# Optimization experiments

Hardware: AMD Instinct MI355X
Metric: run time of the kernel (lower is better)

The kernel has to match this reference:

```python
import jax, jax.numpy as jnp
import numpy as np

N, MA, F, NF = 512, 64, 128, 16
UPDATE_RATIO = 0.1
DECAY = 1.0
EPS = 1e-12  # avoids NaN grad of sqrt at self-distance 0 (torch diagonal is masked out by exp anyway)


def setup_inputs() -> dict:
    key = jax.random.key(0)
    ks = jax.random.split(key, 8)
    z = jax.random.randint(ks[0], (N, MA), 0, 10, dtype=jnp.int64) if jax.config.jax_enable_x64 else jax.random.randint(ks[0], (N, MA), 0, 10, dtype=jnp.int32)
    # pad last few atoms of each molecule with -1 to exercise the mask
    z = z.at[:, MA - 8:].set(-1)
    r = jax.random.normal(ks[1], (N, MA, 3), dtype=jnp.float32) * 3.0
    h = jax.random.normal(ks[2], (N, MA, F), dtype=jnp.float32)
    distances = jnp.linspace(0.5, 6.0, NF, dtype=jnp.float32)
    widths = jax.random.uniform(ks[3], (NF,), dtype=jnp.float32) * 0.5 + 0.5  # keep sigma > 0
    din = F * (1 + NF)  # 2176
    W1 = jax.random.normal(ks[4], (din, 512), dtype=jnp.float32) * (1.0 / np.sqrt(din))
    b1 = jnp.zeros((512,), dtype=jnp.float32)
    W2 = jax.random.normal(ks[5], (512, F), dtype=jnp.float32) * (1.0 / np.sqrt(512.0))
    b2 = jnp.zeros((F,), dtype=jnp.float32)
    return {"z": z, "r": r, "h": h, "distances": distances, "widths": widths,
            "W1": W1, "b1": b1, "W2": W2, "b2": b2}


def reference(z, r, h, distances, widths, W1, b1, W2, b2):
    n, ma = z.shape
    nf = distances.shape[0]
    # pairwise distance: (n, ma, ma)
    dv = r[:, :, None, :] - r[:, None, :, :]
    d = jnp.sqrt(jnp.sum(dv * dv, axis=-1) + EPS)
    mu = distances.reshape(1, nf, 1, 1)
    sigma = widths.reshape(1, nf, 1, 1)
    mask1 = (z > -1).astype(h.dtype)                      # (n, ma)
    pair_mask = mask1[:, :, None] * mask1[:, None, :]     # (n, ma, ma)
    # Gaussian RBF scores, masked: (n, nf, ma, ma)
    w = pair_mask[:, None] * jnp.exp(-((d[:, None] - mu) ** 2) / sigma) * 5.0
    # aggregate neighbor features: (n, ma, nf, F) -> (n, ma, nf*F)
    u = jnp.einsum('nfab,nbc->nafc', w, h).reshape(n, ma, nf * h.shape[-1])
    v = jnp.concatenate([h, u], axis=2)                   # (n, ma, F*(1+nf))
    v = jax.nn.silu(v @ W1 + b1) @ W2 + b2                # MLP 'net'
    h_new = h + v * UPDATE_RATIO * DECAY * mask1[:, :, None]
    return (z, r, h_new)
```

## Files before the change

### kernel.cpp

```cpp
#include <hip/hip_runtime.h>

#define MA 64
#define F 128
#define NF 16
#define HID 512
#define LDUB 144
#define LDWB 144
#define LDT1B 1040
#define UB0 0
#define UB1 9216
#define WL0 18432
#define WL1 27648

typedef float  float4v __attribute__((ext_vector_type(4)));
typedef short  short8  __attribute__((ext_vector_type(8)));
typedef int    int8v   __attribute__((ext_vector_type(8)));

static __device__ __forceinline__ unsigned int pack2bf(float x, float y) {
    unsigned int a = __float_as_uint(x) + 0x8000u;
    unsigned int b = __float_as_uint(y) + 0x8000u;
    return __builtin_amdgcn_perm(b, a, 0x07060302u);
}
static __device__ __forceinline__ unsigned short f2bf1(float x) {
    return (unsigned short)((__float_as_uint(x) + 0x8000u) >> 16);
}
static __device__ __forceinline__ unsigned int pk4fp8(float a, float b, float c, float d) {
    int p = __builtin_amdgcn_cvt_pk_fp8_f32(a, b, 0, false);
    p = __builtin_amdgcn_cvt_pk_fp8_f32(c, d, p, true);
    return (unsigned int)p;
}

#define LGKM_BAR() do {                                        \
    asm volatile("s_waitcnt lgkmcnt(0)" ::: "memory");         \
    __builtin_amdgcn_s_barrier();                              \
    asm volatile("" ::: "memory");                             \
} while (0)

__global__ void pack_frags(const float* __restrict__ W1, const float* __restrict__ W2,
                           unsigned char* __restrict__ w1p, unsigned short* __restrict__ w2p) {
    int gid  = blockIdx.x * 4 + (threadIdx.x >> 6);
    int lane = threadIdx.x & 63;
    int arow = lane & 15;
    int kq   = lane >> 4;
    if (gid < 544) {
        int kt = gid >> 5, jt = gid & 31;
        const float* base = W1 + (size_t)(kt * 128 + kq * 32) * HID + jt * 16 + arow;
        unsigned int o[8];
        #pragma unroll
        for (int p = 0; p < 8; p++)
            o[p] = pk4fp8(base[(p * 4 + 0) * HID], base[(p * 4 + 1) * HID],
                          base[(p * 4 + 2) * HID], base[(p * 4 + 3) * HID]);
        unsigned char* dst = w1p + ((size_t)gid * 64 + lane) * 32;
        *(uint4*)dst        = (uint4){o[0], o[1], o[2], o[3]};
        *(uint4*)(dst + 16) = (uint4){o[4], o[5], o[6], o[7]};
    } else if (gid < 544 + 128) {
        int g2 = gid - 544;
        int kt = g2 >> 3, mt = g2 & 7;
        const float* base = W2 + (size_t)(kt * 32 + kq * 8) * F + mt * 16 + arow;
        short8 o;
        #pragma unroll
        for (int j = 0; j < 8; j++) o[j] = (short)f2bf1(base[j * F]);
        *(short8*)(w2p + ((size_t)g2 * 64 + lane) * 8) = o;
    }
}

__launch_bounds__(512, 2)
__global__ void node_conv_mfma(const int* __restrict__ z, const float* __restrict__ rr,
        const float* __restrict__ h, const float* __restrict__ dist,
        const float* __restrict__ wid, const float* __restrict__ b1,
        const float* __restrict__ b2,
        const unsigned char* __restrict__ w1p, const unsigned short* __restrict__ w2p,
        float* __restrict__ out) {
    const int n = blockIdx.x;
    const int tid = threadIdx.x;
    const int lane = tid & 63;
    const int wave = tid >> 6;
    const int arow = lane & 15;
    const int quad = lane >> 4;
    const int kgrp = quad * 8;

    __shared__ __attribute__((aligned(16))) unsigned char lds[66560];
    __shared__ float r_lds[MA][5];

    const int N = gridDim.x;
    const float* hg = h + (size_t)n * MA * F;

    if (tid < MA) {
        int zi = z[n * MA + tid];
        out[(size_t)n * MA + tid] = (float)zi;
        r_lds[tid][0] = rr[(n * MA + tid) * 3 + 0];
        r_lds[tid][1] = rr[(n * MA + tid) * 3 + 1];
        r_lds[tid][2] = rr[(n * MA + tid) * 3 + 2];
        r_lds[tid][3] = (zi > -1) ? 1.0f : 0.0f;
    }
    if (tid < MA * 3)
        out[(size_t)N * MA + (size_t)n * MA * 3 + tid] = rr[(size_t)n * MA * 3 + tid];

    for (int i = tid; i < MA * F / 4; i += 512) {
        float4 v = ((const float4*)hg)[i];
        int a = i >> 5, c4 = (i & 31) * 4;
        *(unsigned int*)&lds[UB0 + a * LDUB + c4] = pk4fp8(v.x, v.y, v.z, v.w);
    }
    short8 ah[2];
    {
        int c = wave * 16 + arow;
        #pragma unroll
        for (int ks2 = 0; ks2 < 2; ks2++)
            #pragma unroll
            for (int j = 0; j < 8; j++)
                ah[ks2][j] = (short)f2bf1(hg[(size_t)(ks2 * 32 + kgrp + j) * F + c]);
    }
    __syncthreads();

    const int wa = tid >> 3;
    const int wb0 = (tid & 7) * 8;
    float dpre[8];
    {
        float ax = r_lds[wa][0], ay = r_lds[wa][1], az = r_lds[wa][2];
        float am = r_lds[wa][3];
        #pragma unroll
        for (int j = 0; j < 8; j++) {
            float dx = ax - r_lds[wb0 + j][0];
            float dy = ay - r_lds[wb0 + j][1];
            float dz = az - r_lds[wb0 + j][2];
            float d = sqrtf(dx * dx + dy * dy + dz * dz + 1e-12f);
            float mm = am * r_lds[wb0 + j][3];
            dpre[j] = d + (1.0f - mm) * 1e4f;
        }
    }

    {
        float mu = dist[0];
        float isg = 1.0f / wid[0];
        float e[8];
        #pragma unroll
        for (int j = 0; j < 8; j++) {
            float t = dpre[j] - mu;
            e[j] = 5.0f * __expf(-t * t * isg);
        }
        uint4 wp = { pack2bf(e[0], e[1]), pack2bf(e[2], e[3]),
                     pack2bf(e[4], e[5]), pack2bf(e[6], e[7]) };
        *(uint4*)&lds[WL0 + wa * LDWB + wb0 * 2] = wp;
    }
    int8v afr[4];
    #pragma unroll
    for (int mt = 0; mt < 4; mt++)
        afr[mt] = *(const int8v*)(w1p + ((size_t)((wave * 4 + mt) * 64 + lane)) * 32);
    LGKM_BAR();

    const float4v zf = {0.f, 0.f, 0.f, 0.f};
    float4v acc[4][4];
    #pragma unroll
    for (int i = 0; i < 4; i++)
        #pragma unroll
        for (int jv = 0; jv < 4; jv++) acc[i][jv] = zf;

    for (int f = 0; f <= NF; f++) {
        const int sel = f & 1;
        const int ubR = sel ? UB1 : UB0;
        const int ubW = sel ? UB0 : UB1;
        const int wlR = sel ? WL1 : WL0;
        const int wlW = sel ? WL0 : WL1;

        #pragma unroll
        for (int at = 0; at < 4; at++) {
            int8v bfr = *(const int8v*)&lds[ubR + (at * 16 + arow) * LDUB + quad * 32];
            #pragma unroll
            for (int mt = 0; mt < 4; mt++)
                acc[mt][at] = __builtin_amdgcn_mfma_scale_f32_16x16x128_f8f6f4(
                    afr[mt], bfr, acc[mt][at], 0, 0, 0, 127, 0, 127);
        }

        if (f < NF) {
            const unsigned char* pN = w1p + ((size_t)(((f + 1) * 32 + wave * 4) * 64 + lane)) * 32;
            #pragma unroll
            for (int mt = 0; mt < 4; mt++) afr[mt] = *(const int8v*)(pN + mt * 2048);

            float4v ud[4];
            #pragma unroll
            for (int at = 0; at < 4; at++) ud[at] = zf;
            #pragma unroll
            for (int ks2 = 0; ks2 < 2; ks2++)
                #pragma unroll
                for (int at = 0; at < 4; at++) {
                    short8 bw = *(const short8*)&lds[wlR + (at * 16 + arow) * LDWB + (ks2 * 32 + kgrp) * 2];
                    ud[at] = __builtin_amdgcn_mfma_f32_16x16x32_bf16(ah[ks2], bw, ud[at], 0, 0, 0);
                }
            #pragma unroll
            for (int at = 0; at < 4; at++) {
                unsigned int udp = pk4fp8(ud[at][0], ud[at][1], ud[at][2], ud[at][3]);
                *(unsigned int*)&lds[ubW + (at * 16 + arow) * LDUB + wave * 16 + quad * 4] = udp;
            }

            if (f <= NF - 2) {
                float mu = dist[f + 1];
                float isg = 1.0f / wid[f + 1];
                float e[8];
                #pragma unroll
                for (int j = 0; j < 8; j++) {
                    float t = dpre[j] - mu;
                    e[j] = 5.0f * __expf(-t * t * isg);
                }
                uint4 wp = { pack2bf(e[0], e[1]), pack2bf(e[2], e[3]),
                             pack2bf(e[4], e[5]), pack2bf(e[6], e[7]) };
                *(uint4*)&lds[wlW + wa * LDWB + wb0 * 2] = wp;
            }
        }
        LGKM_BAR();
    }

    float4 b1v[4];
    #pragma unroll
    for (int mt = 0; mt < 4; mt++)
        b1v[mt] = *(const float4*)&b1[wave * 64 + mt * 16 + quad * 4];

    short8 aw2r[16];
    #pragma unroll
    for (int ks = 0; ks < 16; ks++)
        aw2r[ks] = *(const short8*)(w2p + ((size_t)(ks * 8 + wave) * 64 + lane) * 8);

    #pragma unroll
    for (int mt = 0; mt < 4; mt++) {
        #pragma unroll
        for (int at = 0; at < 4; at++) {
            float xs[4];
            #pragma unroll
            for (int r = 0; r < 4; r++) {
                float x = acc[mt][at][r] + ((const float*)&b1v[mt])[r];
                xs[r] = x / (1.0f + __expf(-x));
            }
            uint2 pv = { pack2bf(xs[0], xs[1]), pack2bf(xs[2], xs[3]) };
            *(uint2*)&lds[(at * 16 + arow) * LDT1B + (wave * 64 + mt * 16 + quad * 4) * 2] = pv;
        }
    }
    LGKM_BAR();

    float4v g2[4];
    const float4v zf2 = {0.f, 0.f, 0.f, 0.f};
    #pragma unroll
    for (int n2 = 0; n2 < 4; n2++) g2[n2] = zf2;
    #pragma unroll
    for (int ks = 0; ks < 16; ks++) {
        #pragma unroll
        for (int n2 = 0; n2 < 4; n2++) {
            short8 bt = *(const short8*)&lds[(n2 * 16 + arow) * LDT1B + (ks * 32 + kgrp) * 2];
            g2[n2] = __builtin_amdgcn_mfma_f32_16x16x32_bf16(aw2r[ks], bt, g2[n2], 0, 0, 0);
        }
    }

    float* outh = out + (size_t)N * MA * 4 + (size_t)n * MA * F;
    const int c0 = wave * 16 + quad * 4;
    float4 b2v = *(const float4*)&b2[c0];
    #pragma unroll
    for (int n2 = 0; n2 < 4; n2++) {
        int a = n2 * 16 + arow;
        float m = r_lds[a][3] * 0.1f;
        float4 hv = *(const float4*)&hg[a * F + c0];
        float4 res;
        res.x = hv.x + (g2[n2][0] + b2v.x) * m;
        res.y = hv.y + (g2[n2][1] + b2v.y) * m;
        res.z = hv.z + (g2[n2][2] + b2v.z) * m;
        res.w = hv.w + (g2[n2][3] + b2v.w) * m;
        *(float4*)&outh[(size_t)a * F + c0] = res;
    }
}

extern "C" void kernel_launch(void* const* d_in, const int* in_sizes, int n_in,
                              void* d_out, int out_size, void* d_ws, size_t ws_size,
                              hipStream_t stream) {
    const int*   z    = (const int*)d_in[0];
    const float* rr   = (const float*)d_in[1];
    const float* h    = (const float*)d_in[2];
    const float* dist = (const float*)d_in[3];
    const float* wid  = (const float*)d_in[4];
    const float* W1   = (const float*)d_in[5];
    const float* b1   = (const float*)d_in[6];
    const float* W2   = (const float*)d_in[7];
    const float* b2   = (const float*)d_in[8];
    float* out = (float*)d_out;

    int Nmol = in_sizes[0] / MA;

    unsigned char*  w1p = (unsigned char*)d_ws;
    unsigned short* w2p = (unsigned short*)(w1p + (size_t)544 * 64 * 32);

    pack_frags<<<168, 256, 0, stream>>>(W1, W2, w1p, w2p);
    node_conv_mfma<<<Nmol, 512, 0, stream>>>(z, rr, h, dist, wid, b1, b2, w1p, w2p, out);
}
```

Measured before the change: 145.7 us.

## Cut register pressure by streaming weight fragments and raising the launch-bounds occupancy target

Raises the launch-bounds minimum blocks per CU from 2 to 4, which caps VGPRs per thread. To fit that cap, W1 FP8 fragments are now held two at a time (reloaded mid-iteration), the bias-free W2 fragments are double-buffered per k-step instead of 16 preloaded registers, and the feature-aggregation MFMAs are processed in pairs. The goal is more resident waves to hide latency. The risk is that the ~66 KB LDS per block still limits residency, so extra global loads inside the hot loop and possible spills could cost more than the occupancy gain.

After: 174.6 us. 19.9% more time.

```diff
diff --git a/kernel.cpp b/kernel.cpp
--- a/kernel.cpp
+++ b/kernel.cpp
@@ -64,7 +64,7 @@
     }
 }
 
-__launch_bounds__(512, 2)
+__launch_bounds__(512, 4)
 __global__ void node_conv_mfma(const int* __restrict__ z, const float* __restrict__ rr,
         const float* __restrict__ h, const float* __restrict__ dist,
         const float* __restrict__ wid, const float* __restrict__ b1,
@@ -142,10 +142,12 @@
                      pack2bf(e[4], e[5]), pack2bf(e[6], e[7]) };
         *(uint4*)&lds[WL0 + wa * LDWB + wb0 * 2] = wp;
     }
-    int8v afr[4];
-    #pragma unroll
-    for (int mt = 0; mt < 4; mt++)
-        afr[mt] = *(const int8v*)(w1p + ((size_t)((wave * 4 + mt) * 64 + lane)) * 32);
+    int8v afrA, afrB;
+    {
+        const unsigned char* p0 = w1p + ((size_t)((wave * 4) * 64 + lane)) * 32;
+        afrA = *(const int8v*)p0;
+        afrB = *(const int8v*)(p0 + 2048);
+    }
     LGKM_BAR();
 
     const float4v zf = {0.f, 0.f, 0.f, 0.f};
@@ -161,35 +163,46 @@
         const int ubW = sel ? UB0 : UB1;
         const int wlR = sel ? WL1 : WL0;
         const int wlW = sel ? WL0 : WL1;
+        const unsigned char* pseg = w1p + ((size_t)((f * 32 + wave * 4) * 64 + lane)) * 32;
 
         #pragma unroll
         for (int at = 0; at < 4; at++) {
             int8v bfr = *(const int8v*)&lds[ubR + (at * 16 + arow) * LDUB + quad * 32];
-            #pragma unroll
-            for (int mt = 0; mt < 4; mt++)
-                acc[mt][at] = __builtin_amdgcn_mfma_scale_f32_16x16x128_f8f6f4(
-                    afr[mt], bfr, acc[mt][at], 0, 0, 0, 127, 0, 127);
+            acc[0][at] = __builtin_amdgcn_mfma_scale_f32_16x16x128_f8f6f4(
+                afrA, bfr, acc[0][at], 0, 0, 0, 127, 0, 127);
+            acc[1][at] = __builtin_amdgcn_mfma_scale_f32_16x16x128_f8f6f4(
+                afrB, bfr, acc[1][at], 0, 0, 0, 127, 0, 127);
+        }
+        afrA = *(const int8v*)(pseg + 2 * 2048);
+        afrB = *(const int8v*)(pseg + 3 * 2048);
+        #pragma unroll
+        for (int at = 0; at < 4; at++) {
+            int8v bfr = *(const int8v*)&lds[ubR + (at * 16 + arow) * LDUB + quad * 32];
+            acc[2][at] = __builtin_amdgcn_mfma_scale_f32_16x16x128_f8f6f4(
+                afrA, bfr, acc[2][at], 0, 0, 0, 127, 0, 127);
+            acc[3][at] = __builtin_amdgcn_mfma_scale_f32_16x16x128_f8f6f4(
+                afrB, bfr, acc[3][at], 0, 0, 0, 127, 0, 127);
         }
 
         if (f < NF) {
             const unsigned char* pN = w1p + ((size_t)(((f + 1) * 32 + wave * 4) * 64 + lane)) * 32;
+            afrA = *(const int8v*)pN;
+            afrB = *(const int8v*)(pN + 2048);
+
             #pragma unroll
-            for (int mt = 0; mt < 4; mt++) afr[mt] = *(const int8v*)(pN + mt * 2048);
-
-            float4v ud[4];
-            #pragma unroll
-            for (int at = 0; at < 4; at++) ud[at] = zf;
-            #pragma unroll
-            for (int ks2 = 0; ks2 < 2; ks2++)
+            for (int atp = 0; atp < 2; atp++) {
+                float4v ud0 = zf, ud1 = zf;
                 #pragma unroll
-                for (int at = 0; at < 4; at++) {
-                    short8 bw = *(const short8*)&lds[wlR + (at * 16 + arow) * LDWB + (ks2 * 32 + kgrp) * 2];
-                    ud[at] = __builtin_amdgcn_mfma_f32_16x16x32_bf16(ah[ks2], bw, ud[at], 0, 0, 0);
+                for (int ks2 = 0; ks2 < 2; ks2++) {
+                    short8 bw0 = *(const short8*)&lds[wlR + ((atp * 2 + 0) * 16 + arow) * LDWB + (ks2 * 32 + kgrp) * 2];
+                    ud0 = __builtin_amdgcn_mfma_f32_16x16x32_bf16(ah[ks2], bw0, ud0, 0, 0, 0);
+                    short8 bw1 = *(const short8*)&lds[wlR + ((atp * 2 + 1) * 16 + arow) * LDWB + (ks2 * 32 + kgrp) * 2];
+                    ud1 = __builtin_amdgcn_mfma_f32_16x16x32_bf16(ah[ks2], bw1, ud1, 0, 0, 0);
                 }
-            #pragma unroll
-            for (int at = 0; at < 4; at++) {
-                unsigned int udp = pk4fp8(ud[at][0], ud[at][1], ud[at][2], ud[at][3]);
-                *(unsigned int*)&lds[ubW + (at * 16 + arow) * LDUB + wave * 16 + quad * 4] = udp;
+                unsigned int u0 = pk4fp8(ud0[0], ud0[1], ud0[2], ud0[3]);
+                unsigned int u1 = pk4fp8(ud1[0], ud1[1], ud1[2], ud1[3]);
+                *(unsigned int*)&lds[ubW + ((atp * 2 + 0) * 16 + arow) * LDUB + wave * 16 + quad * 4] = u0;
+                *(unsigned int*)&lds[ubW + ((atp * 2 + 1) * 16 + arow) * LDUB + wave * 16 + quad * 4] = u1;
             }
 
             if (f <= NF - 2) {
@@ -214,11 +227,6 @@
     for (int mt = 0; mt < 4; mt++)
         b1v[mt] = *(const float4*)&b1[wave * 64 + mt * 16 + quad * 4];
 
-    short8 aw2r[16];
-    #pragma unroll
-    for (int ks = 0; ks < 16; ks++)
-        aw2r[ks] = *(const short8*)(w2p + ((size_t)(ks * 8 + wave) * 64 + lane) * 8);
-
     #pragma unroll
     for (int mt = 0; mt < 4; mt++) {
         #pragma unroll
@@ -236,15 +244,25 @@
     LGKM_BAR();
 
     float4v g2[4];
-    const float4v zf2 = {0.f, 0.f, 0.f, 0.f};
-    #pragma unroll
-    for (int n2 = 0; n2 < 4; n2++) g2[n2] = zf2;
-    #pragma unroll
-    for (int ks = 0; ks < 16; ks++) {
+    #pragma unroll
+    for (int n2 = 0; n2 < 4; n2++) g2[n2] = zf;
+
+    short8 awA = *(const short8*)(w2p + ((size_t)(wave) * 64 + lane) * 8);
+    #pragma unroll
+    for (int ks2 = 0; ks2 < 8; ks2++) {
+        const int k1 = 2 * ks2 + 1;
+        short8 awB = *(const short8*)(w2p + ((size_t)(k1 * 8 + wave) * 64 + lane) * 8);
         #pragma unroll
         for (int n2 = 0; n2 < 4; n2++) {
-            short8 bt = *(const short8*)&lds[(n2 * 16 + arow) * LDT1B + (ks * 32 + kgrp) * 2];
-            g2[n2] = __builtin_amdgcn_mfma_f32_16x16x32_bf16(aw2r[ks], bt, g2[n2], 0, 0, 0);
+            short8 bt = *(const short8*)&lds[(n2 * 16 + arow) * LDT1B + ((2 * ks2) * 32 + kgrp) * 2];
+            g2[n2] = __builtin_amdgcn_mfma_f32_16x16x32_bf16(awA, bt, g2[n2], 0, 0, 0);
+        }
+        const int k2 = (ks2 < 7) ? 2 * ks2 + 2 : 0;
+        awA = *(const short8*)(w2p + ((size_t)(k2 * 8 + wave) * 64 + lane) * 8);
+        #pragma unroll
+        for (int n2 = 0; n2 < 4; n2++) {
+            short8 bt = *(const short8*)&lds[(n2 * 16 + arow) * LDT1B + ((2 * ks2 + 1) * 32 + kgrp) * 2];
+            g2[n2] = __builtin_amdgcn_mfma_f32_16x16x32_bf16(awB, bt, g2[n2], 0, 0, 0);
         }
     }
 
```
